# Performance work log

Measured on AMD Instinct MI355X. Metric: run time of the kernel, lower is better.

Reference implementation:

```python
import jax, jax.numpy as jnp
import numpy as np

WS = 8          # window size M
SHIFT = WS // 2 # cyclic shift
HEADS = 8


def _rel_pos_index(ws):
    # (ws*ws, ws*ws) indices into the (2ws-1)^2 bias table
    coords = np.stack(np.meshgrid(np.arange(ws), np.arange(ws), indexing='ij'), 0).reshape(2, -1)
    rel = coords[:, :, None] - coords[:, None, :]          # (2, N, N)
    rel = rel.transpose(1, 2, 0) + (ws - 1)                # shift to [0, 2ws-2]
    return rel[..., 0] * (2 * ws - 1) + rel[..., 1]        # (N, N)


def _shift_mask(H, W, ws, shift):
    # standard Swin attention mask for shifted windows: (nWin, N, N)
    img = np.zeros((H, W), dtype=np.int32)
    cnt = 0
    for hs in (slice(0, -ws), slice(-ws, -shift), slice(-shift, None)):
        for wsl in (slice(0, -ws), slice(-ws, -shift), slice(-shift, None)):
            img[hs, wsl] = cnt
            cnt += 1
    mw = img.reshape(H // ws, ws, W // ws, ws).transpose(0, 2, 1, 3).reshape(-1, ws * ws)
    diff = mw[:, None, :] - mw[:, :, None]
    return np.where(diff != 0, -100.0, 0.0).astype(np.float32)


def setup_inputs() -> dict:
    key = jax.random.key(0)
    ks = jax.random.split(key, 6)
    B, C, H, W = 32, 256, 64, 64
    return {
        'x': jax.random.normal(ks[0], (B, C, H, W), jnp.float32),
        'w_qkv': jax.random.normal(ks[1], (C, 3 * C), jnp.float32) * (C ** -0.5),
        'b_qkv': jnp.zeros((3 * C,), jnp.float32),
        'w_o': jax.random.normal(ks[2], (C, C), jnp.float32) * (C ** -0.5),
        'b_o': jnp.zeros((C,), jnp.float32),
        'rel_bias_table': jax.random.normal(ks[3], ((2 * WS - 1) ** 2, HEADS), jnp.float32) * 0.02,
    }


def reference(x, w_qkv, b_qkv, w_o, b_o, rel_bias_table):
    B, C, H, W = x.shape
    ws, shift, heads = WS, SHIFT, HEADS
    dh = C // heads
    nH, nW = H // ws, W // ws
    nWin, N = nH * nW, ws * ws

    rel_idx = jnp.asarray(_rel_pos_index(ws))                 # (N, N) int
    mask = jnp.asarray(_shift_mask(H, W, ws, shift))          # (nWin, N, N)

    # cyclic shift
    xs = jnp.roll(x, (-shift, -shift), axis=(2, 3))
    # window partition: (B, C, H, W) -> (B, nWin, N, C)
    xw = xs.reshape(B, C, nH, ws, nW, ws).transpose(0, 2, 4, 3, 5, 1).reshape(B, nWin, N, C)

    qkv = xw @ w_qkv + b_qkv                                  # (B, nWin, N, 3C)
    qkv = qkv.reshape(B, nWin, N, 3, heads, dh)
    q = qkv[..., 0, :, :].transpose(0, 1, 3, 2, 4)            # (B, nWin, h, N, dh)
    k = qkv[..., 1, :, :].transpose(0, 1, 3, 2, 4)
    v = qkv[..., 2, :, :].transpose(0, 1, 3, 2, 4)

    attn = jnp.einsum('bwhnd,bwhmd->bwhnm', q, k) * (dh ** -0.5)
    bias = rel_bias_table[rel_idx]                            # (N, N, heads)
    attn = attn + bias.transpose(2, 0, 1)[None, None]         # add rel pos bias
    attn = attn + mask[None, :, None]                         # add shift mask
    attn = jax.nn.softmax(attn, axis=-1)

    out = jnp.einsum('bwhnm,bwhmd->bwhnd', attn, v)           # (B, nWin, h, N, dh)
    out = out.transpose(0, 1, 3, 2, 4).reshape(B, nWin, N, C)
    out = out @ w_o + b_o

    # window reverse: (B, nWin, N, C) -> (B, C, H, W)
    out = out.reshape(B, nH, nW, ws, ws, C).transpose(0, 5, 1, 3, 2, 4).reshape(B, C, H, W)
    # reverse cyclic shift
    return jnp.roll(out, (shift, shift), axis=(2, 3))
```

## Files before the change

### kernel.cpp

```cpp
#include <hip/hip_runtime.h>
#include <stdint.h>

typedef __attribute__((ext_vector_type(8))) short short8;
typedef __attribute__((ext_vector_type(4))) float floatx4;
typedef unsigned short u16;

#define MFMA16(a,b,c) __builtin_amdgcn_mfma_f32_16x16x32_bf16((a),(b),(c),0,0,0)

__device__ __forceinline__ u16 f2b(float f){
  unsigned int i; __builtin_memcpy(&i,&f,4); i += 0x7FFFu + ((i>>16)&1u); return (u16)(i>>16);
}
__device__ __forceinline__ int regid(int p){ return (p<56)?0:((p<60)?1:2); }

#define SCO 16896
#define LDS_ELEMS 35328

__global__ void prep_w(const float* __restrict__ wqkv, const float* __restrict__ wo,
                       u16* __restrict__ wqkvT, u16* __restrict__ woT){
  int idx = blockIdx.x*256 + threadIdx.x;
  if(idx < 768*256){ int n = idx>>8, k = idx&255; wqkvT[idx] = f2b(wqkv[k*768 + n]); }
  else { int j = idx - 768*256; int n = j>>8, k = j&255; woT[j] = f2b(wo[k*256 + n]); }
}

__global__ __launch_bounds__(256,2) void swmsa_fused(
    const float* __restrict__ x, const u16* __restrict__ wqkvT, const float* __restrict__ bqkv,
    const u16* __restrict__ woT, const float* __restrict__ bo, const float* __restrict__ table,
    float* __restrict__ out)
{
  extern __shared__ u16 lds[];
  const int tid  = threadIdx.x;
  const int wave = tid>>6, lane = tid&63;
  const int quad = lane>>4, colid = lane&15;
  const int blk = blockIdx.x;
  const int b = blk>>6, win = blk&63, wy = win>>3, wx = win&7;
  const size_t imgbase = (size_t)b*256*4096;
  const int w0 = wx*8+4;
  const floatx4 fzero = {0.f,0.f,0.f,0.f};
  u16* sc = lds + SCO + wave*4608;

  for(int i=0;i<2;++i){
    int unit = tid + 256*i;
    int cg = unit>>3, ty = unit&7;
    int hs = (wy*8+ty+4)&63;
    u16 vv[4][8];
    #pragma unroll
    for(int cc=0;cc<4;++cc){
      const float* src = x + imgbase + (size_t)(cg*4+cc)*4096 + (size_t)hs*64;
      floatx4 lo, hi;
      if(wx<7){ lo = *(const floatx4*)(src+w0); hi = *(const floatx4*)(src+w0+4); }
      else    { lo = *(const floatx4*)(src+60); hi = *(const floatx4*)(src); }
      #pragma unroll
      for(int t=0;t<4;++t){ vv[cc][t]=f2b(lo[t]); vv[cc][4+t]=f2b(hi[t]); }
    }
    #pragma unroll
    for(int t=0;t<8;++t){
      uint64_t pk = (uint64_t)vv[0][t] | ((uint64_t)vv[1][t]<<16)
                  | ((uint64_t)vv[2][t]<<32) | ((uint64_t)vv[3][t]<<48);
      *(uint64_t*)&lds[(ty*8+t)*264 + cg*4] = pk;
    }
  }
  __syncthreads();

  short8 aq2[2][4], bk2[2][4], bv2[2][2][2];
  for(int ci=0; ci<3; ++ci){
    const int col0 = (ci*4 + wave)*64;
    floatx4 acc[4][4];
    #pragma unroll
    for(int mt=0;mt<4;++mt)
      #pragma unroll
      for(int nt=0;nt<4;++nt) acc[mt][nt] = fzero;
    for(int k0=0;k0<256;k0+=32){
      short8 af[4], bfr[4];
      #pragma unroll
      for(int mt=0;mt<4;++mt) af[mt]  = *(const short8*)&lds[(mt*16+colid)*264 + k0 + quad*8];
      #pragma unroll
      for(int nt=0;nt<4;++nt) bfr[nt] = *(const short8*)&wqkvT[(size_t)(col0+nt*16+colid)*256 + k0 + quad*8];
      #pragma unroll
      for(int mt=0;mt<4;++mt)
        #pragma unroll
        for(int nt=0;nt<4;++nt) acc[mt][nt] = MFMA16(af[mt], bfr[nt], acc[mt][nt]);
    }
    #pragma unroll
    for(int nt=0;nt<4;++nt){
      int cloc = nt*16 + colid;
      float bias = bqkv[col0 + cloc];
      #pragma unroll
      for(int mt=0;mt<4;++mt)
        #pragma unroll
        for(int r=0;r<4;++r){
          int row = mt*16 + quad*4 + r;
          u16 bvv = f2b(acc[mt][nt][r] + bias);
          if(ci<2) sc[row*72 + cloc] = bvv;
          else     sc[cloc*72 + row] = bvv;
        }
    }
    if(ci==0){
      #pragma unroll
      for(int hi=0;hi<2;++hi)
        #pragma unroll
        for(int mt=0;mt<4;++mt)
          aq2[hi][mt] = *(const short8*)&sc[(mt*16+colid)*72 + hi*32 + quad*8];
    } else if(ci==1){
      #pragma unroll
      for(int hi=0;hi<2;++hi)
        #pragma unroll
        for(int mt=0;mt<4;++mt)
          bk2[hi][mt] = *(const short8*)&sc[(mt*16+colid)*72 + hi*32 + quad*8];
    } else {
      #pragma unroll
      for(int hi=0;hi<2;++hi)
        #pragma unroll
        for(int n2=0;n2<2;++n2)
          #pragma unroll
          for(int kc=0;kc<2;++kc)
            bv2[hi][n2][kc] = *(const short8*)&sc[(hi*32+n2*16+colid)*72 + kc*32 + quad*8];
    }
  }
  __syncthreads();

  const float scale = 0.17677669529663687f;
  #pragma unroll
  for(int hi=0; hi<2; ++hi){
    const int h = wave*2 + hi;
    floatx4 s[4][4];
    #pragma unroll
    for(int mt=0;mt<4;++mt)
      #pragma unroll
      for(int nt=0;nt<4;++nt) s[mt][nt] = MFMA16(aq2[hi][mt], bk2[hi][nt], fzero);
    int cntk[4], kys[4], kxs[4];
    #pragma unroll
    for(int nt=0;nt<4;++nt){
      int col = nt*16 + colid;
      kys[nt] = col>>3; kxs[nt] = col&7;
      cntk[nt] = regid(wy*8 + kys[nt])*3 + regid(wx*8 + kxs[nt]);
    }
    #pragma unroll
    for(int mt=0;mt<4;++mt)
      #pragma unroll
      for(int r=0;r<4;++r){
        int row = mt*16 + quad*4 + r;
        int ty = row>>3, tx = row&7;
        int cntq = regid(wy*8+ty)*3 + regid(wx*8+tx);
        #pragma unroll
        for(int nt=0;nt<4;++nt){
          int rel = (ty - kys[nt] + 7)*15 + (tx - kxs[nt] + 7);
          float add = table[rel*8 + h] + ((cntq==cntk[nt]) ? 0.f : -100.f);
          s[mt][nt][r] = s[mt][nt][r]*scale + add;
        }
      }
    #pragma unroll
    for(int mt=0;mt<4;++mt)
      #pragma unroll
      for(int r=0;r<4;++r){
        float mx = s[mt][0][r];
        #pragma unroll
        for(int nt=1;nt<4;++nt) mx = fmaxf(mx, s[mt][nt][r]);
        #pragma unroll
        for(int d=1; d<16; d<<=1) mx = fmaxf(mx, __shfl_xor(mx, d));
        float e[4], sum = 0.f;
        #pragma unroll
        for(int nt=0;nt<4;++nt){ e[nt] = __expf(s[mt][nt][r]-mx); sum += e[nt]; }
        #pragma unroll
        for(int d=1; d<16; d<<=1) sum += __shfl_xor(sum, d);
        float inv = 1.0f/sum;
        int row = mt*16 + quad*4 + r;
        #pragma unroll
        for(int nt=0;nt<4;++nt) sc[row*72 + nt*16 + colid] = f2b(e[nt]*inv);
      }
    floatx4 o[4][2];
    #pragma unroll
    for(int mt=0;mt<4;++mt){ o[mt][0]=fzero; o[mt][1]=fzero; }
    #pragma unroll
    for(int kc=0;kc<2;++kc){
      short8 ap[4];
      #pragma unroll
      for(int mt=0;mt<4;++mt) ap[mt] = *(const short8*)&sc[(mt*16+colid)*72 + kc*32 + quad*8];
      #pragma unroll
      for(int mt=0;mt<4;++mt)
        #pragma unroll
        for(int n2=0;n2<2;++n2) o[mt][n2] = MFMA16(ap[mt], bv2[hi][n2][kc], o[mt][n2]);
    }
    #pragma unroll
    for(int n2=0;n2<2;++n2){
      int c = h*32 + n2*16 + colid;
      #pragma unroll
      for(int mt=0;mt<4;++mt)
        #pragma unroll
        for(int r=0;r<4;++r){
          int row = mt*16 + quad*4 + r;
          lds[row*264 + c] = f2b(o[mt][n2][r]);
        }
    }
  }
  __syncthreads();

  float* oTh = (float*)(lds + SCO);
  for(int np=0; np<2; ++np){
    const int col0 = np*128 + wave*32;
    floatx4 acc[4][2];
    #pragma unroll
    for(int mt=0;mt<4;++mt){ acc[mt][0]=fzero; acc[mt][1]=fzero; }
    for(int k0=0;k0<256;k0+=32){
      short8 ay[4], bw[2];
      #pragma unroll
      for(int mt=0;mt<4;++mt) ay[mt] = *(const short8*)&lds[(mt*16+colid)*264 + k0 + quad*8];
      #pragma unroll
      for(int n2=0;n2<2;++n2) bw[n2] = *(const short8*)&woT[(size_t)(col0+n2*16+colid)*256 + k0 + quad*8];
      #pragma unroll
      for(int mt=0;mt<4;++mt)
        #pragma unroll
        for(int n2=0;n2<2;++n2) acc[mt][n2] = MFMA16(ay[mt], bw[n2], acc[mt][n2]);
    }
    #pragma unroll
    for(int n2=0;n2<2;++n2){
      int cl = wave*32 + n2*16 + colid;
      float bias = bo[np*128 + cl];
      #pragma unroll
      for(int mt=0;mt<4;++mt)
        #pragma unroll
        for(int r=0;r<4;++r)
          oTh[cl*72 + mt*16 + quad*4 + r] = acc[mt][n2][r] + bias;
    }
    __syncthreads();
    for(int i=0;i<4;++i){
      int rid = tid + 256*i;
      int cl = rid>>3, ty = rid&7;
      floatx4 lo  = *(const floatx4*)&oTh[cl*72 + ty*8];
      floatx4 hi2 = *(const floatx4*)&oTh[cl*72 + ty*8 + 4];
      int hd = (wy*8+ty+4)&63;
      float* dst = out + imgbase + (size_t)(np*128+cl)*4096 + (size_t)hd*64;
      if(wx<7){ *(floatx4*)(dst+w0) = lo; *(floatx4*)(dst+w0+4) = hi2; }
      else    { *(floatx4*)(dst+60) = lo; *(floatx4*)(dst)      = hi2; }
    }
    if(np==0) __syncthreads();
  }
}

extern "C" void kernel_launch(void* const* d_in, const int* in_sizes, int n_in,
                              void* d_out, int out_size, void* d_ws, size_t ws_size,
                              hipStream_t stream) {
  const float* x     = (const float*)d_in[0];
  const float* wqkv  = (const float*)d_in[1];
  const float* bqkv  = (const float*)d_in[2];
  const float* wo    = (const float*)d_in[3];
  const float* bo    = (const float*)d_in[4];
  const float* table = (const float*)d_in[5];
  float* out = (float*)d_out;

  u16* wqkvT = (u16*)d_ws;
  u16* woT   = wqkvT + 768*256;

  prep_w<<<1024, 256, 0, stream>>>(wqkv, wo, wqkvT, woT);

  (void)hipFuncSetAttribute((const void*)swmsa_fused,
                            hipFuncAttributeMaxDynamicSharedMemorySize, LDS_ELEMS*2);
  swmsa_fused<<<2048, 256, LDS_ELEMS*2, stream>>>(x, wqkvT, bqkv, woT, bo, table, out);
}
```

Baseline: 501.1 us.

## Shrink per-wave LDS scratch to fit three blocks per CU and remap blocks across XCDs

Halves the per-wave scratch buffer by staging Q/K/V and the softmax probabilities in 32-column halves, and holds half of the probabilities packed in registers. The output projection is split into four 64-column passes so the smaller float staging area is enough. Together these cut LDS from about 70KB to 52KB so launch bounds can ask for three blocks per CU. Blocks are also remapped so that neighbouring windows of one image share an XCD, for better L2 locality of x and out. The cost is more syncthreads, more, smaller LDS round trips and higher register pressure under the tighter launch bound.

```diff
diff --git a/kernel.cpp b/kernel.cpp
--- a/kernel.cpp
+++ b/kernel.cpp
@@ -4,16 +4,17 @@
 typedef __attribute__((ext_vector_type(8))) short short8;
 typedef __attribute__((ext_vector_type(4))) float floatx4;
 typedef unsigned short u16;
+typedef unsigned int u32;
 
 #define MFMA16(a,b,c) __builtin_amdgcn_mfma_f32_16x16x32_bf16((a),(b),(c),0,0,0)
 
 __device__ __forceinline__ u16 f2b(float f){
-  unsigned int i; __builtin_memcpy(&i,&f,4); i += 0x7FFFu + ((i>>16)&1u); return (u16)(i>>16);
+  u32 i; __builtin_memcpy(&i,&f,4); i += 0x7FFFu + ((i>>16)&1u); return (u16)(i>>16);
 }
 __device__ __forceinline__ int regid(int p){ return (p<56)?0:((p<60)?1:2); }
 
 #define SCO 16896
-#define LDS_ELEMS 35328
+#define LDS_ELEMS 26112
 
 __global__ void prep_w(const float* __restrict__ wqkv, const float* __restrict__ wo,
                        u16* __restrict__ wqkvT, u16* __restrict__ woT){
@@ -22,7 +23,7 @@
   else { int j = idx - 768*256; int n = j>>8, k = j&255; woT[j] = f2b(wo[k*256 + n]); }
 }
 
-__global__ __launch_bounds__(256,2) void swmsa_fused(
+__global__ __launch_bounds__(256,3) void swmsa_fused(
     const float* __restrict__ x, const u16* __restrict__ wqkvT, const float* __restrict__ bqkv,
     const u16* __restrict__ woT, const float* __restrict__ bo, const float* __restrict__ table,
     float* __restrict__ out)
@@ -31,12 +32,15 @@
   const int tid  = threadIdx.x;
   const int wave = tid>>6, lane = tid&63;
   const int quad = lane>>4, colid = lane&15;
-  const int blk = blockIdx.x;
-  const int b = blk>>6, win = blk&63, wy = win>>3, wx = win&7;
+  const int bi = blockIdx.x;
+  const int xcd = bi & 7, j = bi >> 3;
+  const int r0 = ((j >> 3) << 3) | xcd;
+  const int wx = j & 7;
+  const int b = r0 >> 3, wy = r0 & 7;
   const size_t imgbase = (size_t)b*256*4096;
   const int w0 = wx*8+4;
   const floatx4 fzero = {0.f,0.f,0.f,0.f};
-  u16* sc = lds + SCO + wave*4608;
+  u16* sc = lds + SCO + wave*2304;
 
   for(int i=0;i<2;++i){
     int unit = tid + 256*i;
@@ -62,8 +66,9 @@
   __syncthreads();
 
   short8 aq2[2][4], bk2[2][4], bv2[2][2][2];
-  for(int ci=0; ci<3; ++ci){
-    const int col0 = (ci*4 + wave)*64;
+  for(int t3=0; t3<3; ++t3){
+    const int cc = 2 - t3;
+    const int col0 = (cc*4 + wave)*64;
     floatx4 acc[4][4];
     #pragma unroll
     for(int mt=0;mt<4;++mt)
@@ -81,39 +86,34 @@
         for(int nt=0;nt<4;++nt) acc[mt][nt] = MFMA16(af[mt], bfr[nt], acc[mt][nt]);
     }
     #pragma unroll
-    for(int nt=0;nt<4;++nt){
-      int cloc = nt*16 + colid;
-      float bias = bqkv[col0 + cloc];
-      #pragma unroll
-      for(int mt=0;mt<4;++mt)
-        #pragma unroll
-        for(int r=0;r<4;++r){
-          int row = mt*16 + quad*4 + r;
-          u16 bvv = f2b(acc[mt][nt][r] + bias);
-          if(ci<2) sc[row*72 + cloc] = bvv;
-          else     sc[cloc*72 + row] = bvv;
-        }
-    }
-    if(ci==0){
-      #pragma unroll
-      for(int hi=0;hi<2;++hi)
+    for(int hf=0; hf<2; ++hf){
+      #pragma unroll
+      for(int nt2=0; nt2<2; ++nt2){
+        int nt = hf*2 + nt2;
+        float bias = bqkv[col0 + nt*16 + colid];
         #pragma unroll
         for(int mt=0;mt<4;++mt)
-          aq2[hi][mt] = *(const short8*)&sc[(mt*16+colid)*72 + hi*32 + quad*8];
-    } else if(ci==1){
-      #pragma unroll
-      for(int hi=0;hi<2;++hi)
-        #pragma unroll
-        for(int mt=0;mt<4;++mt)
-          bk2[hi][mt] = *(const short8*)&sc[(mt*16+colid)*72 + hi*32 + quad*8];
-    } else {
-      #pragma unroll
-      for(int hi=0;hi<2;++hi)
+          #pragma unroll
+          for(int rr=0;rr<4;++rr){
+            int row = mt*16 + quad*4 + rr;
+            u16 bvv = f2b(acc[mt][nt][rr] + bias);
+            if(cc==2) sc[(nt2*16+colid)*72 + row] = bvv;
+            else      sc[row*36 + nt2*16 + colid] = bvv;
+          }
+      }
+      if(cc==2){
         #pragma unroll
         for(int n2=0;n2<2;++n2)
           #pragma unroll
           for(int kc=0;kc<2;++kc)
-            bv2[hi][n2][kc] = *(const short8*)&sc[(hi*32+n2*16+colid)*72 + kc*32 + quad*8];
+            bv2[hf][n2][kc] = *(const short8*)&sc[(n2*16+colid)*72 + kc*32 + quad*8];
+      } else if(cc==1){
+        #pragma unroll
+        for(int mt=0;mt<4;++mt) bk2[hf][mt] = *(const short8*)&sc[(mt*16+colid)*36 + quad*8];
+      } else {
+        #pragma unroll
+        for(int mt=0;mt<4;++mt) aq2[hf][mt] = *(const short8*)&sc[(mt*16+colid)*36 + quad*8];
+      }
     }
   }
   __syncthreads();
@@ -137,44 +137,56 @@
     #pragma unroll
     for(int mt=0;mt<4;++mt)
       #pragma unroll
-      for(int r=0;r<4;++r){
-        int row = mt*16 + quad*4 + r;
+      for(int rr=0;rr<4;++rr){
+        int row = mt*16 + quad*4 + rr;
         int ty = row>>3, tx = row&7;
         int cntq = regid(wy*8+ty)*3 + regid(wx*8+tx);
         #pragma unroll
         for(int nt=0;nt<4;++nt){
           int rel = (ty - kys[nt] + 7)*15 + (tx - kxs[nt] + 7);
           float add = table[rel*8 + h] + ((cntq==cntk[nt]) ? 0.f : -100.f);
-          s[mt][nt][r] = s[mt][nt][r]*scale + add;
+          s[mt][nt][rr] = s[mt][nt][rr]*scale + add;
         }
       }
-    #pragma unroll
-    for(int mt=0;mt<4;++mt)
-      #pragma unroll
-      for(int r=0;r<4;++r){
-        float mx = s[mt][0][r];
-        #pragma unroll
-        for(int nt=1;nt<4;++nt) mx = fmaxf(mx, s[mt][nt][r]);
+    u32 gpk[4][4];
+    #pragma unroll
+    for(int mt=0;mt<4;++mt)
+      #pragma unroll
+      for(int rr=0;rr<4;++rr){
+        float mx = s[mt][0][rr];
+        #pragma unroll
+        for(int nt=1;nt<4;++nt) mx = fmaxf(mx, s[mt][nt][rr]);
         #pragma unroll
         for(int d=1; d<16; d<<=1) mx = fmaxf(mx, __shfl_xor(mx, d));
         float e[4], sum = 0.f;
         #pragma unroll
-        for(int nt=0;nt<4;++nt){ e[nt] = __expf(s[mt][nt][r]-mx); sum += e[nt]; }
+        for(int nt=0;nt<4;++nt){ e[nt] = __expf(s[mt][nt][rr]-mx); sum += e[nt]; }
         #pragma unroll
         for(int d=1; d<16; d<<=1) sum += __shfl_xor(sum, d);
         float inv = 1.0f/sum;
-        int row = mt*16 + quad*4 + r;
-        #pragma unroll
-        for(int nt=0;nt<4;++nt) sc[row*72 + nt*16 + colid] = f2b(e[nt]*inv);
+        int row = mt*16 + quad*4 + rr;
+        sc[row*36 + colid]      = f2b(e[0]*inv);
+        sc[row*36 + 16 + colid] = f2b(e[1]*inv);
+        gpk[mt][rr] = (u32)f2b(e[2]*inv) | ((u32)f2b(e[3]*inv) << 16);
       }
     floatx4 o[4][2];
     #pragma unroll
     for(int mt=0;mt<4;++mt){ o[mt][0]=fzero; o[mt][1]=fzero; }
     #pragma unroll
     for(int kc=0;kc<2;++kc){
+      if(kc==1){
+        #pragma unroll
+        for(int mt=0;mt<4;++mt)
+          #pragma unroll
+          for(int rr=0;rr<4;++rr){
+            int row = mt*16 + quad*4 + rr;
+            sc[row*36 + colid]      = (u16)(gpk[mt][rr] & 0xffffu);
+            sc[row*36 + 16 + colid] = (u16)(gpk[mt][rr] >> 16);
+          }
+      }
       short8 ap[4];
       #pragma unroll
-      for(int mt=0;mt<4;++mt) ap[mt] = *(const short8*)&sc[(mt*16+colid)*72 + kc*32 + quad*8];
+      for(int mt=0;mt<4;++mt) ap[mt] = *(const short8*)&sc[(mt*16+colid)*36 + quad*8];
       #pragma unroll
       for(int mt=0;mt<4;++mt)
         #pragma unroll
@@ -186,53 +198,48 @@
       #pragma unroll
       for(int mt=0;mt<4;++mt)
         #pragma unroll
-        for(int r=0;r<4;++r){
-          int row = mt*16 + quad*4 + r;
-          lds[row*264 + c] = f2b(o[mt][n2][r]);
-        }
+        for(int rr=0;rr<4;++rr)
+          lds[(mt*16+quad*4+rr)*264 + c] = f2b(o[mt][n2][rr]);
     }
   }
   __syncthreads();
 
-  float* oTh = (float*)(lds + SCO);
-  for(int np=0; np<2; ++np){
-    const int col0 = np*128 + wave*32;
-    floatx4 acc[4][2];
-    #pragma unroll
-    for(int mt=0;mt<4;++mt){ acc[mt][0]=fzero; acc[mt][1]=fzero; }
+  float* oQ = (float*)(lds + SCO);
+  for(int np=0; np<4; ++np){
+    const int col0 = np*64 + wave*16;
+    floatx4 acc[4];
+    #pragma unroll
+    for(int mt=0;mt<4;++mt) acc[mt] = fzero;
     for(int k0=0;k0<256;k0+=32){
-      short8 ay[4], bw[2];
+      short8 ay[4], bw;
       #pragma unroll
       for(int mt=0;mt<4;++mt) ay[mt] = *(const short8*)&lds[(mt*16+colid)*264 + k0 + quad*8];
-      #pragma unroll
-      for(int n2=0;n2<2;++n2) bw[n2] = *(const short8*)&woT[(size_t)(col0+n2*16+colid)*256 + k0 + quad*8];
-      #pragma unroll
-      for(int mt=0;mt<4;++mt)
-        #pragma unroll
-        for(int n2=0;n2<2;++n2) acc[mt][n2] = MFMA16(ay[mt], bw[n2], acc[mt][n2]);
-    }
-    #pragma unroll
-    for(int n2=0;n2<2;++n2){
-      int cl = wave*32 + n2*16 + colid;
-      float bias = bo[np*128 + cl];
-      #pragma unroll
-      for(int mt=0;mt<4;++mt)
-        #pragma unroll
-        for(int r=0;r<4;++r)
-          oTh[cl*72 + mt*16 + quad*4 + r] = acc[mt][n2][r] + bias;
+      bw = *(const short8*)&woT[(size_t)(col0+colid)*256 + k0 + quad*8];
+      #pragma unroll
+      for(int mt=0;mt<4;++mt) acc[mt] = MFMA16(ay[mt], bw, acc[mt]);
+    }
+    if(np) __syncthreads();
+    {
+      float bias = bo[col0 + colid];
+      int cl = wave*16 + colid;
+      #pragma unroll
+      for(int mt=0;mt<4;++mt)
+        #pragma unroll
+        for(int rr=0;rr<4;++rr)
+          oQ[cl*72 + mt*16 + quad*4 + rr] = acc[mt][rr] + bias;
     }
     __syncthreads();
-    for(int i=0;i<4;++i){
-      int rid = tid + 256*i;
-      int cl = rid>>3, ty = rid&7;
-      floatx4 lo  = *(const floatx4*)&oTh[cl*72 + ty*8];
-      floatx4 hi2 = *(const floatx4*)&oTh[cl*72 + ty*8 + 4];
+    #pragma unroll
+    for(int i=0;i<2;++i){
+      int unit = tid + 256*i;
+      int cl = unit>>3, ty = unit&7;
+      floatx4 lo  = *(const floatx4*)&oQ[cl*72 + ty*8];
+      floatx4 hi2 = *(const floatx4*)&oQ[cl*72 + ty*8 + 4];
       int hd = (wy*8+ty+4)&63;
-      float* dst = out + imgbase + (size_t)(np*128+cl)*4096 + (size_t)hd*64;
+      float* dst = out + imgbase + (size_t)(np*64+cl)*4096 + (size_t)hd*64;
       if(wx<7){ *(floatx4*)(dst+w0) = lo; *(floatx4*)(dst+w0+4) = hi2; }
       else    { *(floatx4*)(dst+60) = lo; *(floatx4*)(dst)      = hi2; }
     }
-    if(np==0) __syncthreads();
   }
 }
 
```

Result: faster. 484.3 us (-3.3%).
